# Kernel optimization log

Hardware: AMD Instinct MI355X
Metric: run time of the kernel (lower is better)

## Reference

```python
import jax, jax.numpy as jnp
import numpy as np

DIM = 128; D_STATE = 16; D_CONV = 4; EXPAND = 2
D_INNER = DIM * EXPAND            # 256
DT_RANK = (DIM + 15) // 16        # 8
B, H, W = 2, 56, 56


def _ln(x, w, b):
    m = jnp.mean(x, -1, keepdims=True)
    v = jnp.var(x, -1, keepdims=True)
    return (x - m) * jax.lax.rsqrt(v + 1e-5) * w + b


def _mamba(x, in_w, conv_w, conv_b, xproj_w, dt_w, dt_b, A_log, Dp, out_w):
    # x: (B, L, DIM)
    Bb, L, _ = x.shape
    xz = x @ in_w.T                                   # (B,L,2*D_INNER)
    xi, z = jnp.split(xz, 2, axis=-1)
    # causal depthwise conv1d (pad left d_conv-1, truncate to L)
    xc = jnp.transpose(xi, (0, 2, 1))                 # (B,D_INNER,L)
    xc = jax.lax.conv_general_dilated(
        xc, conv_w, (1,), [(D_CONV - 1, 0)],
        dimension_numbers=('NCH', 'OIH', 'NCH'),
        feature_group_count=D_INNER) + conv_b[None, :, None]
    xs = jax.nn.silu(jnp.transpose(xc, (0, 2, 1)))    # (B,L,D_INNER)
    dbl = xs @ xproj_w.T                              # (B,L,DT_RANK+2*D_STATE)
    dt = jax.nn.softplus(dbl[..., :DT_RANK] @ dt_w.T + dt_b)   # (B,L,D_INNER)
    Bc = dbl[..., DT_RANK:DT_RANK + D_STATE]          # (B,L,D_STATE)
    Cc = dbl[..., DT_RANK + D_STATE:]                 # (B,L,D_STATE)
    A = -jnp.exp(A_log)                               # (D_INNER,D_STATE)
    dA = jnp.exp(dt[..., None] * A)                   # (B,L,D_INNER,D_STATE)
    dBu = (dt * xs)[..., None] * Bc[:, :, None, :]    # (B,L,D_INNER,D_STATE)

    def step(h, inp):
        a, bu, c = inp
        h = a * h + bu                                # (B,D_INNER,D_STATE)
        return h, jnp.einsum('bdn,bn->bd', h, c)

    h0 = jnp.zeros((Bb, D_INNER, D_STATE), x.dtype)
    _, ys = jax.lax.scan(step, h0, (jnp.moveaxis(dA, 1, 0),
                                    jnp.moveaxis(dBu, 1, 0),
                                    jnp.moveaxis(Cc, 1, 0)))
    y = jnp.moveaxis(ys, 0, 1) + xs * Dp              # (B,L,D_INNER)
    y = y * jax.nn.silu(z)
    return y @ out_w.T                                # (B,L,DIM)


def _forward(x, norm_h_w, norm_h_b, norm_v_w, norm_v_b,
             dw_w, dw_b, pw_w, pw_b,
             h_in_w, h_conv_w, h_conv_b, h_xproj_w, h_dt_w, h_dt_b, h_A_log, h_D, h_out_w,
             v_in_w, v_conv_w, v_conv_b, v_xproj_w, v_dt_w, v_dt_b, v_A_log, v_D, v_out_w,
             ca_fc1_w, ca_fc2_w):
    Bb, C, Hh, Ww = x.shape
    # local branch: depthwise 3x3 + GELU + 1x1
    lf = jax.lax.conv_general_dilated(
        x, dw_w, (1, 1), [(1, 1), (1, 1)],
        dimension_numbers=('NCHW', 'OIHW', 'NCHW'),
        feature_group_count=C) + dw_b[None, :, None, None]
    lf = jax.nn.gelu(lf, approximate=False)
    lf = jnp.einsum('bchw,oc->bohw', lf, pw_w[:, :, 0, 0]) + pw_b[None, :, None, None]
    # horizontal scan: row-major tokens
    xh = _ln(x.reshape(Bb, C, Hh * Ww).transpose(0, 2, 1), norm_h_w, norm_h_b)
    oh = _mamba(xh, h_in_w, h_conv_w, h_conv_b, h_xproj_w, h_dt_w, h_dt_b,
                h_A_log, h_D, h_out_w)
    oh = oh.transpose(0, 2, 1).reshape(Bb, C, Hh, Ww)
    # vertical scan: column-major tokens
    xv = _ln(jnp.transpose(x, (0, 1, 3, 2)).reshape(Bb, C, Ww * Hh).transpose(0, 2, 1),
             norm_v_w, norm_v_b)
    ov = _mamba(xv, v_in_w, v_conv_w, v_conv_b, v_xproj_w, v_dt_w, v_dt_b,
                v_A_log, v_D, v_out_w)
    ov = jnp.transpose(ov.transpose(0, 2, 1).reshape(Bb, C, Ww, Hh), (0, 1, 3, 2))
    fused = oh + ov + lf
    # channel attention
    y = jnp.mean(fused, axis=(2, 3))                  # (B,C)
    y = jax.nn.sigmoid(jax.nn.relu(y @ ca_fc1_w.T) @ ca_fc2_w.T)
    return fused * y[:, :, None, None] + x


def setup_inputs() -> dict:
    key = jax.random.key(0)
    ks = iter(jax.random.split(key, 64))
    def nrm(shape, scale):
        return jax.random.normal(next(ks), shape, jnp.float32) * scale
    d = {}
    d['x'] = nrm((B, DIM, H, W), 1.0)
    d['norm_h_w'] = jnp.ones((DIM,), jnp.float32); d['norm_h_b'] = jnp.zeros((DIM,), jnp.float32)
    d['norm_v_w'] = jnp.ones((DIM,), jnp.float32); d['norm_v_b'] = jnp.zeros((DIM,), jnp.float32)
    d['dw_w'] = nrm((DIM, 1, 3, 3), 1.0 / 3.0)
    d['dw_b'] = jnp.zeros((DIM,), jnp.float32)
    d['pw_w'] = nrm((DIM, DIM, 1, 1), DIM ** -0.5)
    d['pw_b'] = jnp.zeros((DIM,), jnp.float32)
    for p in ('h', 'v'):
        d[p + '_in_w'] = nrm((2 * D_INNER, DIM), DIM ** -0.5)
        d[p + '_conv_w'] = nrm((D_INNER, 1, D_CONV), D_CONV ** -0.5)
        d[p + '_conv_b'] = jnp.zeros((D_INNER,), jnp.float32)
        d[p + '_xproj_w'] = nrm((DT_RANK + 2 * D_STATE, D_INNER), D_INNER ** -0.5)
        d[p + '_dt_w'] = nrm((D_INNER, DT_RANK), DT_RANK ** -0.5)
        d[p + '_dt_b'] = jnp.full((D_INNER,), -2.0, jnp.float32)  # small positive dt
        d[p + '_A_log'] = jnp.log(jnp.tile(jnp.arange(1, D_STATE + 1, dtype=jnp.float32), (D_INNER, 1)))
        d[p + '_D'] = jnp.ones((D_INNER,), jnp.float32)
        d[p + '_out_w'] = nrm((DIM, D_INNER), D_INNER ** -0.5)
    d['ca_fc1_w'] = nrm((DIM // 4, DIM), DIM ** -0.5)
    d['ca_fc2_w'] = nrm((DIM, DIM // 4), (DIM // 4) ** -0.5)
    return d


def reference(x, norm_h_w, norm_h_b, norm_v_w, norm_v_b,
              dw_w, dw_b, pw_w, pw_b,
              h_in_w, h_conv_w, h_conv_b, h_xproj_w, h_dt_w, h_dt_b, h_A_log, h_D, h_out_w,
              v_in_w, v_conv_w, v_conv_b, v_xproj_w, v_dt_w, v_dt_b, v_A_log, v_D, v_out_w,
              ca_fc1_w, ca_fc2_w):
    return _forward(x, norm_h_w, norm_h_b, norm_v_w, norm_v_b,
                    dw_w, dw_b, pw_w, pw_b,
                    h_in_w, h_conv_w, h_conv_b, h_xproj_w, h_dt_w, h_dt_b, h_A_log, h_D, h_out_w,
                    v_in_w, v_conv_w, v_conv_b, v_xproj_w, v_dt_w, v_dt_b, v_A_log, v_D, v_out_w,
                    ca_fc1_w, ca_fc2_w)
```

## Files before the change

kernel.cpp:

```cpp
#include <hip/hip_runtime.h>
#include <hip/hip_bf16.h>

typedef __hip_bfloat16 bf16;
__device__ __forceinline__ float b2f(bf16 v){ return __bfloat162float(v); }
__device__ __forceinline__ bf16 f2b(float v){ return __float2bfloat16(v); }

typedef __attribute__((ext_vector_type(8))) short frag_ab;
typedef __attribute__((ext_vector_type(4))) float frag_cd;
typedef __attribute__((ext_vector_type(4))) short short4v;

__device__ __forceinline__ frag_ab ld_frag_2xb64(const bf16* p){
  union { frag_ab f; short4v h[2]; } u;
  u.h[0] = *reinterpret_cast<const short4v*>(p);
  u.h[1] = *reinterpret_cast<const short4v*>(p+4);
  return u.f;
}

#define LLEN 3136
#define BATCH 2
#define NCHUNK 49
#define LC 64

__global__ void k_front(const float* __restrict__ x, const float* __restrict__ dww,
                        const float* __restrict__ dwb, bf16* __restrict__ tmp,
                        const float* nhw_, const float* nhb_, const float* nvw_,
                        const float* nvb_, bf16* __restrict__ xln,
                        float* __restrict__ YMEAN){
  int blk = blockIdx.x;
  int tid = threadIdx.x;
  if (blk < 1024){
    int bc = blk & 255;
    int seg = blk >> 8;
    int c = bc & 127;
    if (bc == 0 && seg == 0 && tid < 256) YMEAN[tid] = 0.f;
    const float* xp = x + (size_t)bc*LLEN;
    float w[9];
    #pragma unroll
    for (int i=0;i<9;i++) w[i] = dww[c*9+i];
    float bias = dwb[c];
    int pstart = seg * 784;
    for (int p = pstart + tid; p < pstart + 784; p += 256){
      int i = p/56, j = p%56;
      float acc = bias;
      #pragma unroll
      for (int a=0;a<3;a++){
        int ii = i + a - 1;
        if (ii < 0 || ii >= 56) continue;
        #pragma unroll
        for (int bb=0;bb<3;bb++){
          int jj = j + bb - 1;
          if (jj < 0 || jj >= 56) continue;
          acc += w[a*3+bb] * xp[ii*56+jj];
        }
      }
      float g = 0.5f*acc*(1.0f + erff(acc*0.70710678118654752f));
      tmp[(size_t)bc*LLEN + p] = f2b(g);
    }
  } else {
    int idx2 = blk - 1024;
    int h = idx2 % 56, b = idx2 / 56;
    __shared__ float sx[128][57];
    __shared__ float smean[56], srstd[56];
    __shared__ float wh[128], bh[128], wv_[128], bv_[128];
    if (tid < 128){ wh[tid]=nhw_[tid]; bh[tid]=nhb_[tid];
                    wv_[tid]=nvw_[tid]; bv_[tid]=nvb_[tid]; }
    for (int idx = tid; idx < 128*56; idx += 256){
      int c = idx / 56, w = idx % 56;
      sx[c][w] = x[((size_t)(b*128+c))*LLEN + h*56 + w];
    }
    __syncthreads();
    if (tid < 56){
      float s=0.f, s2=0.f;
      for (int c=0;c<128;c++){ float v = sx[c][tid]; s+=v; s2+=v*v; }
      float m = s*(1.f/128.f);
      float var = s2*(1.f/128.f) - m*m;
      smean[tid]=m; srstd[tid]=rsqrtf(var+1e-5f);
    }
    __syncthreads();
    bf16* outh = xln;
    bf16* outv = xln + (size_t)BATCH*LLEN*128;
    for (int idx = tid; idx < 56*128; idx += 256){
      int w = idx >> 7, c = idx & 127;
      float v = (sx[c][w]-smean[w])*srstd[w];
      outh[((size_t)b*LLEN + h*56 + w)*128 + c] = f2b(v*wh[c]+bh[c]);
      outv[((size_t)b*LLEN + w*56 + h)*128 + c] = f2b(v*wv_[c]+bv_[c]);
    }
  }
}

__global__ void k_inproj(const bf16* __restrict__ xln, const float* __restrict__ hw,
                         const float* __restrict__ vw, bf16* __restrict__ XI, bf16* __restrict__ Z){
  int dir = blockIdx.z;
  const bf16* A = xln + (size_t)dir*BATCH*LLEN*128;
  const float* W = dir ? vw : hw;
  int m0 = blockIdx.x*64;
  int npair = blockIdx.y*128;
  __shared__ __align__(16) bf16 sA[64][136];
  __shared__ __align__(16) bf16 sW[64][136];
  int tid = threadIdx.x;
  #pragma unroll
  for (int r=0;r<4;r++){
    int idx = tid + r*256;
    int row = idx >> 4, c8 = (idx & 15)*8;
    *reinterpret_cast<float4*>(&sA[row][c8]) =
        *reinterpret_cast<const float4*>(&A[(size_t)(m0+row)*128 + c8]);
  }
  int wv2 = tid >> 6, lane = tid & 63;
  int qd = lane >> 4, mr = lane & 15;
  bf16* dst = (npair < 256) ? XI : Z;
  int nbase0 = npair & 255;
  size_t dslab = (size_t)dir*BATCH*LLEN*256;
  #pragma unroll
  for (int nt=0; nt<2; nt++){
    int n0 = npair + nt*64;
    __syncthreads();
    #pragma unroll
    for (int r=0;r<8;r++){
      int idx = tid + r*256;
      int row = idx >> 5, c4 = (idx & 31)*4;
      float4 w4 = *reinterpret_cast<const float4*>(&W[(size_t)(n0+row)*128 + c4]);
      bf16 t4[4] = {f2b(w4.x), f2b(w4.y), f2b(w4.z), f2b(w4.w)};
      *reinterpret_cast<double*>(&sW[row][c4]) = *reinterpret_cast<double*>(t4);
    }
    __syncthreads();
    frag_cd acc[4] = {};
    #pragma unroll
    for (int k0=0;k0<128;k0+=32){
      frag_ab af = *reinterpret_cast<frag_ab*>(&sA[wv2*16+mr][k0+qd*8]);
      #pragma unroll
      for (int t=0;t<4;t++){
        frag_ab bfr = *reinterpret_cast<frag_ab*>(&sW[t*16+mr][k0+qd*8]);
        acc[t] = __builtin_amdgcn_mfma_f32_16x16x32_bf16(af, bfr, acc[t], 0, 0, 0);
      }
    }
    int nb = nbase0 + nt*64;
    #pragma unroll
    for (int t=0;t<4;t++)
      #pragma unroll
      for (int r=0;r<4;r++){
        int row = m0 + wv2*16 + qd*4 + r;
        int col = nb + t*16 + mr;
        dst[dslab + (size_t)row*256 + col] = f2b(acc[t][r]);
      }
  }
}

__global__ void k_conv(const bf16* __restrict__ XI, const float* hw, const float* hb,
                       const float* vw, const float* vb, bf16* __restrict__ XS2){
  int dir = blockIdx.z;
  int b = blockIdx.y;
  int bd = dir*BATCH + b;
  int l0 = blockIdx.x * 32;
  const bf16* XId = XI + (size_t)bd*LLEN*256;
  const float* cw = dir ? vw : hw;
  const float* cb = dir ? vb : hb;
  __shared__ float sxi[35][256];
  int tid = threadIdx.x;
  for (int r = 0; r < 35; r++){
    int l = l0 - 3 + r;
    sxi[r][tid] = (l >= 0) ? b2f(XId[(size_t)l*256 + tid]) : 0.f;
  }
  __syncthreads();
  float w0=cw[tid*4], w1=cw[tid*4+1], w2=cw[tid*4+2], w3=cw[tid*4+3];
  float bias = cb[tid];
  size_t x2base = ((size_t)bd*16 + (tid>>4))*LLEN;
  int c16 = tid & 15;
  for (int ll=0; ll<32; ll++){
    float acc = bias + w0*sxi[ll][tid] + w1*sxi[ll+1][tid] + w2*sxi[ll+2][tid] + w3*sxi[ll+3][tid];
    float s = acc / (1.f + __expf(-acc));
    XS2[(x2base + l0 + ll)*16 + c16] = f2b(s);
  }
}

__global__ void k_dbl(const bf16* __restrict__ XS2, const float* __restrict__ hx,
                      const float* __restrict__ vx,
                      const float* hdw, const float* vdw, const float* hdb, const float* vdb,
                      bf16* __restrict__ DT2, float* __restrict__ Bf, float* __restrict__ Cf){
  int m0 = blockIdx.x*64;
  int bd = m0 / LLEN;
  int l0m = m0 % LLEN;
  int dirq = bd >> 1;
  const float* W = dirq ? vx : hx;
  __shared__ __align__(16) bf16 sA[64][264];
  __shared__ __align__(16) bf16 sW[48][264];
  __shared__ float sdbl[64][49];
  int tid = threadIdx.x;
  #pragma unroll
  for (int r=0;r<8;r++){
    int idx = tid + r*256;
    int row = idx >> 5, c8 = (idx & 31)*8;
    size_t src = (((size_t)bd*16 + (c8>>4))*LLEN + l0m + row)*16 + (c8&15);
    *reinterpret_cast<float4*>(&sA[row][c8]) =
        *reinterpret_cast<const float4*>(&XS2[src]);
  }
  #pragma unroll
  for (int r=0;r<12;r++){
    int idx = tid + r*256;
    int row = idx >> 6, c4 = (idx & 63)*4;
    bf16 t4[4] = {f2b(0.f), f2b(0.f), f2b(0.f), f2b(0.f)};
    if (row < 40){
      float4 w4 = *reinterpret_cast<const float4*>(&W[(size_t)row*256 + c4]);
      t4[0]=f2b(w4.x); t4[1]=f2b(w4.y); t4[2]=f2b(w4.z); t4[3]=f2b(w4.w);
    }
    *reinterpret_cast<double*>(&sW[row][c4]) = *reinterpret_cast<double*>(t4);
  }
  __syncthreads();
  int wv2 = tid >> 6, lane = tid & 63;
  int qd = lane >> 4, mr = lane & 15;
  frag_cd acc[3] = {};
  #pragma unroll
  for (int k0=0;k0<256;k0+=32){
    frag_ab af = *reinterpret_cast<frag_ab*>(&sA[wv2*16+mr][k0+qd*8]);
    #pragma unroll
    for (int t=0;t<3;t++){
      frag_ab bfr = *reinterpret_cast<frag_ab*>(&sW[t*16+mr][k0+qd*8]);
      acc[t] = __builtin_amdgcn_mfma_f32_16x16x32_bf16(af, bfr, acc[t], 0, 0, 0);
    }
  }
  #pragma unroll
  for (int t=0;t<3;t++)
    #pragma unroll
    for (int r=0;r<4;r++){
      int col = t*16 + mr;
      if (col < 40) sdbl[wv2*16 + qd*4 + r][col] = acc[t][r];
    }
  __syncthreads();
  const float* dtw = dirq ? vdw : hdw;
  const float* dtb = dirq ? vdb : hdb;
  float w8[8];
  #pragma unroll
  for (int r=0;r<8;r++) w8[r] = dtw[tid*8+r];
  float biasv = dtb[tid];
  size_t d2base = ((size_t)bd*16 + (tid>>4))*LLEN + l0m;
  int c16 = tid & 15;
  for (int row=0; row<64; row++){
    float a = biasv;
    #pragma unroll
    for (int r=0;r<8;r++) a += sdbl[row][r]*w8[r];
    float sv = (a > 20.f) ? a : __logf(1.f + __expf(a));
    DT2[(d2base + row)*16 + c16] = f2b(sv);
  }
  #pragma unroll
  for (int r=0;r<8;r++){
    int idx = tid + r*256;
    int row = idx >> 5, o = idx & 31;
    float v = sdbl[row][8+o];
    size_t rr = (size_t)(m0+row)*16;
    if (o < 16) Bf[rr + o] = v;
    else        Cf[rr + (o-16)] = v;
  }
}

__global__ void k_scan1(const bf16* __restrict__ DT2, const bf16* __restrict__ XS2,
                        const float* __restrict__ Bc, const float* hA, const float* vA,
                        float* __restrict__ Pbuf, float* __restrict__ Hbuf){
  int bd = blockIdx.z;
  int g  = blockIdx.y;
  int ck = blockIdx.x;
  int l0 = ck*LC;
  const float* Bd = Bc + (size_t)bd*LLEN*16;
  const float* Alog = (bd >> 1) ? vA : hA;
  int tid = threadIdx.x;
  int dl = tid >> 4, n = tid & 15;
  float A = -__expf(Alog[(g*16+dl)*16+n]);
  __shared__ float sdt[LC][16], sxs[LC][16], sB[LC][16];
  size_t base2 = (((size_t)bd*16 + g)*LLEN + l0)*16;
  #pragma unroll
  for (int r=0;r<4;r++){
    int idx = tid + r*256;
    sdt[idx>>4][idx&15] = b2f(DT2[base2 + idx]);
    sxs[idx>>4][idx&15] = b2f(XS2[base2 + idx]);
    (&sB[0][0])[idx] = Bd[(size_t)l0*16 + idx];
  }
  __syncthreads();
  float h = 0.f, P = 1.f;
  #pragma unroll 8
  for (int i=0;i<LC;i++){
    float a = sdt[i][dl];
    float u = sxs[i][dl];
    float dA = __expf(a * A);
    h = dA*h + (a*u)*sB[i][n];
    P *= dA;
  }
  size_t sidx = (((size_t)bd*16 + g)*NCHUNK + ck)*256 + tid;
  Pbuf[sidx] = P;
  Hbuf[sidx] = h;
}

__global__ void k_scan2(const float* __restrict__ Pbuf, float* __restrict__ Hbuf){
  int q = blockIdx.x;
  int tid = threadIdx.x;
  float carry = 0.f;
  for (int k=0;k<NCHUNK;k++){
    size_t idx = ((size_t)q*NCHUNK + k)*256 + tid;
    float Pv = Pbuf[idx];
    float He = Hbuf[idx];
    Hbuf[idx] = carry;
    carry = Pv*carry + He;
  }
}

__global__ void k_scan3(const bf16* __restrict__ DT2, const bf16* __restrict__ XS2,
                        const float* __restrict__ Bc, const float* __restrict__ Cc,
                        const float* hA, const float* vA,
                        const float* __restrict__ Hbuf, bf16* __restrict__ ys){
  int bd = blockIdx.z;
  int g  = blockIdx.y;
  int ck = blockIdx.x;
  int l0 = ck*LC;
  const float* Bd = Bc + (size_t)bd*LLEN*16;
  const float* Cd = Cc + (size_t)bd*LLEN*16;
  bf16* yd = ys + (size_t)bd*LLEN*256;
  const float* Alog = (bd >> 1) ? vA : hA;
  int tid = threadIdx.x;
  int dl = tid >> 4, n = tid & 15;
  float A = -__expf(Alog[(g*16+dl)*16+n]);
  __shared__ float sdt[LC][16], sxs[LC][16], sB[LC][16], sC[LC][16];
  __shared__ float sp2[16][272];
  size_t base2 = (((size_t)bd*16 + g)*LLEN + l0)*16;
  #pragma unroll
  for (int r=0;r<4;r++){
    int idx = tid + r*256;
    sdt[idx>>4][idx&15] = b2f(DT2[base2 + idx]);
    sxs[idx>>4][idx&15] = b2f(XS2[base2 + idx]);
    (&sB[0][0])[idx] = Bd[(size_t)l0*16 + idx];
    (&sC[0][0])[idx] = Cd[(size_t)l0*16 + idx];
  }
  size_t sidx = (((size_t)bd*16 + g)*NCHUNK + ck)*256 + tid;
  float h = Hbuf[sidx];
  __syncthreads();
  int swz = dl*17 + n;
  int i_local = tid >> 4;
  int c16 = tid & 15;
  int rbase = c16*17;
  for (int i0=0; i0<LC; i0+=16){
    #pragma unroll
    for (int ii=0;ii<16;ii++){
      int i = i0 + ii;
      float a = sdt[i][dl];
      float u = sxs[i][dl];
      float dA = __expf(a * A);
      h = dA*h + (a*u)*sB[i][n];
      sp2[ii][swz] = h * sC[i][n];
    }
    __syncthreads();
    const float* row = &sp2[i_local][rbase];
    float s = 0.f;
    #pragma unroll
    for (int k=0;k<16;k++) s += row[k];
    yd[(size_t)(l0+i0+i_local)*256 + g*16 + c16] = f2b(s);
    __syncthreads();
  }
}

__global__ void k_outgemm(const bf16* __restrict__ ys, const bf16* __restrict__ XS2,
                          const bf16* __restrict__ Z, const float* __restrict__ hD,
                          const float* __restrict__ vD, const float* __restrict__ how,
                          const float* __restrict__ vow, bf16* __restrict__ OD){
  int dir = blockIdx.y;
  size_t slab = (size_t)dir*BATCH*LLEN*256;
  const float* W = dir ? vow : how;
  const float* Dw = dir ? vD : hD;
  bf16* od = OD + (size_t)dir*BATCH*LLEN*128;
  int m0 = blockIdx.x*32;
  int bd = dir*2 + m0/LLEN;
  int lbase = m0 % LLEN;
  __shared__ __align__(16) bf16 sA[32][264];
  __shared__ __align__(16) bf16 sW[64][264];
  int tid = threadIdx.x;
  #pragma unroll
  for (int r=0;r<4;r++){
    int idx = tid + r*256;
    int row = idx >> 5, c8 = (idx & 31)*8;
    size_t e = slab + (size_t)(m0+row)*256 + c8;
    size_t e2 = (((size_t)bd*16 + (c8>>4))*LLEN + lbase + row)*16 + (c8&15);
    bf16 yb[8], xb[8], zb[8], ob[8];
    *reinterpret_cast<float4*>(yb) = *reinterpret_cast<const float4*>(&ys[e]);
    *reinterpret_cast<float4*>(xb) = *reinterpret_cast<const float4*>(&XS2[e2]);
    *reinterpret_cast<float4*>(zb) = *reinterpret_cast<const float4*>(&Z[e]);
    #pragma unroll
    for (int j=0;j<8;j++){
      float Dv = Dw[c8 + j];
      float yv = b2f(yb[j]) + b2f(xb[j])*Dv;
      float zv = b2f(zb[j]);
      ob[j] = f2b(yv * (zv/(1.f+__expf(-zv))));
    }
    *reinterpret_cast<float4*>(&sA[row][c8]) = *reinterpret_cast<float4*>(ob);
  }
  int wv2 = tid >> 6, lane = tid & 63;
  int qd = lane >> 4, mr = lane & 15;
  int msub = wv2 & 1, tpair = (wv2 >> 1)*2;
  #pragma unroll
  for (int nh=0; nh<2; nh++){
    int n0 = nh*64;
    __syncthreads();
    #pragma unroll
    for (int r=0;r<16;r++){
      int idx = tid + r*256;
      int row = idx >> 6, c4 = (idx & 63)*4;
      float4 w4 = *reinterpret_cast<const float4*>(&W[(size_t)(n0+row)*256 + c4]);
      bf16 t4[4] = {f2b(w4.x), f2b(w4.y), f2b(w4.z), f2b(w4.w)};
      *reinterpret_cast<double*>(&sW[row][c4]) = *reinterpret_cast<double*>(t4);
    }
    __syncthreads();
    frag_cd acc[2] = {};
    #pragma unroll
    for (int k0=0;k0<256;k0+=32){
      frag_ab af = *reinterpret_cast<frag_ab*>(&sA[msub*16+mr][k0+qd*8]);
      #pragma unroll
      for (int i=0;i<2;i++){
        frag_ab bfr = *reinterpret_cast<frag_ab*>(&sW[(tpair+i)*16+mr][k0+qd*8]);
        acc[i] = __builtin_amdgcn_mfma_f32_16x16x32_bf16(af, bfr, acc[i], 0, 0, 0);
      }
    }
    #pragma unroll
    for (int i=0;i<2;i++)
      #pragma unroll
      for (int r=0;r<4;r++){
        int row = m0 + msub*16 + qd*4 + r;
        int col = n0 + (tpair+i)*16 + mr;
        od[(size_t)row*128 + col] = f2b(acc[i][r]);
      }
  }
}

__global__ void k_pwcomb(const bf16* __restrict__ tmp, const float* __restrict__ pww,
                         const float* __restrict__ pwb, const bf16* __restrict__ OD,
                         float* __restrict__ fused, float* __restrict__ YMEAN){
  int p0 = blockIdx.x * 64;
  int m0 = blockIdx.y * 64;
  int b  = blockIdx.z;
  const bf16* T = tmp + (size_t)b*128*LLEN;
  const bf16* od0 = OD + (size_t)b*LLEN*128;
  const bf16* od1 = OD + (size_t)(BATCH + b)*LLEN*128;
  __shared__ __align__(16) bf16 sA[64][136];
  __shared__ __align__(16) bf16 sBt[64][132];
  __shared__ float sOD[64][65];
  int tid = threadIdx.x;
  #pragma unroll
  for (int r=0;r<8;r++){
    int idx = tid + r*256;
    int row = idx >> 5, c4 = (idx & 31)*4;
    float4 w4 = *reinterpret_cast<const float4*>(&pww[(size_t)(m0+row)*128 + c4]);
    bf16 t4[4] = {f2b(w4.x), f2b(w4.y), f2b(w4.z), f2b(w4.w)};
    *reinterpret_cast<double*>(&sA[row][c4]) = *reinterpret_cast<double*>(t4);
  }
  #pragma unroll
  for (int r=0;r<8;r++){
    int idx = tid + r*256;
    int c = idx >> 4, p4 = (idx & 15)*4;
    union { double d; bf16 v[4]; } u;
    u.d = *reinterpret_cast<const double*>(&T[(size_t)c*LLEN + p0 + p4]);
    #pragma unroll
    for (int j=0;j<4;j++) sBt[p4+j][c] = u.v[j];
  }
  #pragma unroll
  for (int r=0;r<8;r++){
    int idx = tid + r*256;
    int prow = idx >> 5, mp = (idx & 31)*2;
    int p = p0 + prow;
    int pi = p/56, pj = p%56;
    int pt = pj*56 + pi;
    bf16 a0[2], a1[2];
    *reinterpret_cast<float*>(a0) = *reinterpret_cast<const float*>(&od0[(size_t)p*128 + m0 + mp]);
    *reinterpret_cast<float*>(a1) = *reinterpret_cast<const float*>(&od1[(size_t)pt*128 + m0 + mp]);
    sOD[prow][mp]   = b2f(a0[0]) + b2f(a1[0]);
    sOD[prow][mp+1] = b2f(a0[1]) + b2f(a1[1]);
  }
  __syncthreads();
  int wv2 = tid >> 6, lane = tid & 63;
  int qd = lane >> 4, mr = lane & 15;
  frag_cd acc[4] = {};
  #pragma unroll
  for (int k0=0;k0<128;k0+=32){
    frag_ab af = *reinterpret_cast<frag_ab*>(&sA[wv2*16+mr][k0+qd*8]);
    #pragma unroll
    for (int t=0;t<4;t++){
      frag_ab bfr = ld_frag_2xb64(&sBt[t*16+mr][k0+qd*8]);
      acc[t] = __builtin_amdgcn_mfma_f32_16x16x32_bf16(af, bfr, acc[t], 0, 0, 0);
    }
  }
  #pragma unroll
  for (int r=0;r<4;r++){
    int m = m0 + wv2*16 + qd*4 + r;
    float bias = pwb[m];
    float s = 0.f;
    #pragma unroll
    for (int t=0;t<4;t++){
      int p = p0 + t*16 + mr;
      float val = acc[t][r] + bias + sOD[t*16+mr][m - m0];
      fused[((size_t)b*128 + m)*LLEN + p] = val;
      s += val;
    }
    s += __shfl_xor(s, 1, 16);
    s += __shfl_xor(s, 2, 16);
    s += __shfl_xor(s, 4, 16);
    s += __shfl_xor(s, 8, 16);
    if (mr == 0) atomicAdd(&YMEAN[b*128 + m], s);
  }
}

__global__ void k_final_gate(const float* __restrict__ fused, const float* __restrict__ YMEAN,
                             const float* __restrict__ fc1, const float* __restrict__ fc2,
                             const float* __restrict__ x, float* __restrict__ out){
  int bc = blockIdx.y;
  int b = bc >> 7, c = bc & 127;
  __shared__ float ym[128], s1[32];
  __shared__ float gsh;
  int tid = threadIdx.x;
  if (tid < 128) ym[tid] = YMEAN[b*128 + tid] * (1.f/(float)LLEN);
  __syncthreads();
  if (tid < 32){
    float a = 0.f;
    for (int cc=0;cc<128;cc++) a += ym[cc]*fc1[tid*128+cc];
    s1[tid] = fmaxf(a, 0.f);
  }
  __syncthreads();
  if (tid == 0){
    float a = 0.f;
    #pragma unroll
    for (int j=0;j<32;j++) a += s1[j]*fc2[c*32+j];
    gsh = 1.f/(1.f+__expf(-a));
  }
  __syncthreads();
  float g = gsh;
  int p = blockIdx.x*256 + tid;
  if (p < LLEN){
    size_t i = (size_t)bc*LLEN + p;
    out[i] = fused[i]*g + x[i];
  }
}

extern "C" void kernel_launch(void* const* d_in, const int* in_sizes, int n_in,
                              void* d_out, int out_size, void* d_ws, size_t ws_size,
                              hipStream_t stream) {
  const float* x      = (const float*)d_in[0];
  const float* nhw    = (const float*)d_in[1];
  const float* nhb    = (const float*)d_in[2];
  const float* nvw    = (const float*)d_in[3];
  const float* nvb    = (const float*)d_in[4];
  const float* dww    = (const float*)d_in[5];
  const float* dwb    = (const float*)d_in[6];
  const float* pww    = (const float*)d_in[7];
  const float* pwb    = (const float*)d_in[8];
  const float* h_inw  = (const float*)d_in[9];
  const float* h_cw   = (const float*)d_in[10];
  const float* h_cb   = (const float*)d_in[11];
  const float* h_xw   = (const float*)d_in[12];
  const float* h_dtw  = (const float*)d_in[13];
  const float* h_dtb  = (const float*)d_in[14];
  const float* h_Al   = (const float*)d_in[15];
  const float* h_D    = (const float*)d_in[16];
  const float* h_ow   = (const float*)d_in[17];
  const float* v_inw  = (const float*)d_in[18];
  const float* v_cw   = (const float*)d_in[19];
  const float* v_cb   = (const float*)d_in[20];
  const float* v_xw   = (const float*)d_in[21];
  const float* v_dtw  = (const float*)d_in[22];
  const float* v_dtb  = (const float*)d_in[23];
  const float* v_Al   = (const float*)d_in[24];
  const float* v_D    = (const float*)d_in[25];
  const float* v_ow   = (const float*)d_in[26];
  const float* fc1    = (const float*)d_in[27];
  const float* fc2    = (const float*)d_in[28];

  float* FUSED = (float*)d_out;
  float* out   = (float*)d_out;

  char* base = (char*)d_ws;
  bf16*  XLN   = (bf16*)(base + 1605632);
  bf16*  DT2   = (bf16*)(base + 0);
  bf16*  OD    = (bf16*)(base + 0);
  bf16*  XI    = (bf16*)(base + 6422528);
  bf16*  YS    = (bf16*)(base + 6422528);
  bf16*  Z     = (bf16*)(base + 12845056);
  bf16*  XS2   = (bf16*)(base + 19267584);
  float* Bf    = (float*)(base + 25690112);
  float* Cf    = (float*)(base + 26492928);
  float* Hbuf  = (float*)(base + 27295744);
  float* YMEAN = (float*)(base + 30507008);
  bf16*  TMP   = (bf16*)(base + 30508032);
  float* Pbuf  = (float*)(base + 32113664);

  k_front<<<dim3(1024 + 56*BATCH), dim3(256), 0, stream>>>(x, dww, dwb, TMP,
                                                           nhw, nhb, nvw, nvb, XLN, YMEAN);
  k_inproj<<<dim3(98,4,2), dim3(256), 0, stream>>>(XLN, h_inw, v_inw, XI, Z);
  k_conv<<<dim3(98,BATCH,2), dim3(256), 0, stream>>>(XI, h_cw, h_cb, v_cw, v_cb, XS2);
  k_dbl<<<dim3(196), dim3(256), 0, stream>>>(XS2, h_xw, v_xw, h_dtw, v_dtw, h_dtb, v_dtb,
                                             DT2, Bf, Cf);
  k_scan1<<<dim3(NCHUNK,16,4), dim3(256), 0, stream>>>(DT2, XS2, Bf, h_Al, v_Al, Pbuf, Hbuf);
  k_scan2<<<dim3(64), dim3(256), 0, stream>>>(Pbuf, Hbuf);
  k_scan3<<<dim3(NCHUNK,16,4), dim3(256), 0, stream>>>(DT2, XS2, Bf, Cf, h_Al, v_Al, Hbuf, YS);
  k_outgemm<<<dim3(196,2), dim3(256), 0, stream>>>(YS, XS2, Z, h_D, v_D, h_ow, v_ow, OD);
  k_pwcomb<<<dim3(49,2,BATCH), dim3(256), 0, stream>>>(TMP, pww, pwb, OD, FUSED, YMEAN);
  k_final_gate<<<dim3(13,256), dim3(256), 0, stream>>>(FUSED, YMEAN, fc1, fc2, x, out);
}
```

Baseline: 237.5 us.

## Fuse causal conv+SiLU into x-projection GEMM and restructure final gate kernel

```diff
diff --git a/kernel.cpp b/kernel.cpp
--- a/kernel.cpp
+++ b/kernel.cpp
@@ -145,53 +145,30 @@
   }
 }
 
-__global__ void k_conv(const bf16* __restrict__ XI, const float* hw, const float* hb,
-                       const float* vw, const float* vb, bf16* __restrict__ XS2){
-  int dir = blockIdx.z;
-  int b = blockIdx.y;
-  int bd = dir*BATCH + b;
-  int l0 = blockIdx.x * 32;
-  const bf16* XId = XI + (size_t)bd*LLEN*256;
-  const float* cw = dir ? vw : hw;
-  const float* cb = dir ? vb : hb;
-  __shared__ float sxi[35][256];
-  int tid = threadIdx.x;
-  for (int r = 0; r < 35; r++){
-    int l = l0 - 3 + r;
-    sxi[r][tid] = (l >= 0) ? b2f(XId[(size_t)l*256 + tid]) : 0.f;
-  }
-  __syncthreads();
-  float w0=cw[tid*4], w1=cw[tid*4+1], w2=cw[tid*4+2], w3=cw[tid*4+3];
-  float bias = cb[tid];
-  size_t x2base = ((size_t)bd*16 + (tid>>4))*LLEN;
-  int c16 = tid & 15;
-  for (int ll=0; ll<32; ll++){
-    float acc = bias + w0*sxi[ll][tid] + w1*sxi[ll+1][tid] + w2*sxi[ll+2][tid] + w3*sxi[ll+3][tid];
-    float s = acc / (1.f + __expf(-acc));
-    XS2[(x2base + l0 + ll)*16 + c16] = f2b(s);
-  }
-}
-
-__global__ void k_dbl(const bf16* __restrict__ XS2, const float* __restrict__ hx,
-                      const float* __restrict__ vx,
+__global__ void k_dbl(const bf16* __restrict__ XI,
+                      const float* hcw, const float* hcb, const float* vcw, const float* vcb,
+                      const float* __restrict__ hx, const float* __restrict__ vx,
                       const float* hdw, const float* vdw, const float* hdb, const float* vdb,
-                      bf16* __restrict__ DT2, float* __restrict__ Bf, float* __restrict__ Cf){
+                      bf16* __restrict__ XS2, bf16* __restrict__ DT2,
+                      float* __restrict__ Bf, float* __restrict__ Cf){
   int m0 = blockIdx.x*64;
   int bd = m0 / LLEN;
   int l0m = m0 % LLEN;
   int dirq = bd >> 1;
+  const bf16* XId = XI + (size_t)bd*LLEN*256;
   const float* W = dirq ? vx : hx;
-  __shared__ __align__(16) bf16 sA[64][264];
+  const float* cw = dirq ? vcw : hcw;
+  const float* cb = dirq ? vcb : hcb;
+  __shared__ __align__(16) bf16 sA[67][264];
   __shared__ __align__(16) bf16 sW[48][264];
   __shared__ float sdbl[64][49];
   int tid = threadIdx.x;
-  #pragma unroll
-  for (int r=0;r<8;r++){
-    int idx = tid + r*256;
+  for (int idx = tid; idx < 67*32; idx += 256){
     int row = idx >> 5, c8 = (idx & 31)*8;
-    size_t src = (((size_t)bd*16 + (c8>>4))*LLEN + l0m + row)*16 + (c8&15);
-    *reinterpret_cast<float4*>(&sA[row][c8]) =
-        *reinterpret_cast<const float4*>(&XS2[src]);
+    int l = l0m - 3 + row;
+    float4 v = make_float4(0.f,0.f,0.f,0.f);
+    if (l >= 0) v = *reinterpret_cast<const float4*>(&XId[(size_t)l*256 + c8]);
+    *reinterpret_cast<float4*>(&sA[row][c8]) = v;
   }
   #pragma unroll
   for (int r=0;r<12;r++){
@@ -203,6 +180,24 @@
       t4[0]=f2b(w4.x); t4[1]=f2b(w4.y); t4[2]=f2b(w4.z); t4[3]=f2b(w4.w);
     }
     *reinterpret_cast<double*>(&sW[row][c4]) = *reinterpret_cast<double*>(t4);
+  }
+  __syncthreads();
+  {
+    float w0=cw[tid*4], w1=cw[tid*4+1], w2=cw[tid*4+2], w3=cw[tid*4+3];
+    float cbias = cb[tid];
+    size_t x2base = ((size_t)bd*16 + (tid>>4))*LLEN + l0m;
+    int c16 = tid & 15;
+    float xm3 = b2f(sA[0][tid]), xm2 = b2f(sA[1][tid]), xm1 = b2f(sA[2][tid]);
+    #pragma unroll 4
+    for (int j=0;j<64;j++){
+      float x0 = b2f(sA[j+3][tid]);
+      float acc = cbias + w0*xm3 + w1*xm2 + w2*xm1 + w3*x0;
+      float s = acc / (1.f + __expf(-acc));
+      bf16 sv = f2b(s);
+      sA[j][tid] = sv;
+      XS2[(x2base + j)*16 + c16] = sv;
+      xm3=xm2; xm2=xm1; xm1=x0;
+    }
   }
   __syncthreads();
   int wv2 = tid >> 6, lane = tid & 63;
@@ -291,6 +286,7 @@
   int q = blockIdx.x;
   int tid = threadIdx.x;
   float carry = 0.f;
+  #pragma unroll 7
   for (int k=0;k<NCHUNK;k++){
     size_t idx = ((size_t)q*NCHUNK + k)*256 + tid;
     float Pv = Pbuf[idx];
@@ -503,31 +499,45 @@
 __global__ void k_final_gate(const float* __restrict__ fused, const float* __restrict__ YMEAN,
                              const float* __restrict__ fc1, const float* __restrict__ fc2,
                              const float* __restrict__ x, float* __restrict__ out){
-  int bc = blockIdx.y;
+  int bc = blockIdx.x;
   int b = bc >> 7, c = bc & 127;
   __shared__ float ym[128], s1[32];
   __shared__ float gsh;
   int tid = threadIdx.x;
   if (tid < 128) ym[tid] = YMEAN[b*128 + tid] * (1.f/(float)LLEN);
   __syncthreads();
+  {
+    int o = tid >> 3, part = tid & 7;
+    float a = 0.f;
+    #pragma unroll
+    for (int k=0;k<16;k++) a += ym[part*16 + k] * fc1[o*128 + part*16 + k];
+    a += __shfl_xor(a, 1, 8);
+    a += __shfl_xor(a, 2, 8);
+    a += __shfl_xor(a, 4, 8);
+    if (part == 0) s1[o] = fmaxf(a, 0.f);
+  }
+  __syncthreads();
   if (tid < 32){
-    float a = 0.f;
-    for (int cc=0;cc<128;cc++) a += ym[cc]*fc1[tid*128+cc];
-    s1[tid] = fmaxf(a, 0.f);
-  }
-  __syncthreads();
-  if (tid == 0){
-    float a = 0.f;
-    #pragma unroll
-    for (int j=0;j<32;j++) a += s1[j]*fc2[c*32+j];
-    gsh = 1.f/(1.f+__expf(-a));
+    float a = s1[tid] * fc2[c*32 + tid];
+    a += __shfl_xor(a, 1, 32);
+    a += __shfl_xor(a, 2, 32);
+    a += __shfl_xor(a, 4, 32);
+    a += __shfl_xor(a, 8, 32);
+    a += __shfl_xor(a, 16, 32);
+    if (tid == 0) gsh = 1.f/(1.f+__expf(-a));
   }
   __syncthreads();
   float g = gsh;
-  int p = blockIdx.x*256 + tid;
-  if (p < LLEN){
-    size_t i = (size_t)bc*LLEN + p;
-    out[i] = fused[i]*g + x[i];
+  const float4* f4 = reinterpret_cast<const float4*>(fused) + (size_t)bc*784;
+  const float4* x4 = reinterpret_cast<const float4*>(x) + (size_t)bc*784;
+  float4* o4 = reinterpret_cast<float4*>(out) + (size_t)bc*784;
+  #pragma unroll
+  for (int it=0; it<4; it++){
+    int p = it*256 + tid;
+    if (p < 784){
+      float4 fv = f4[p], xv = x4[p];
+      o4[p] = make_float4(fv.x*g+xv.x, fv.y*g+xv.y, fv.z*g+xv.z, fv.w*g+xv.w);
+    }
   }
 }
 
@@ -585,13 +595,13 @@
   k_front<<<dim3(1024 + 56*BATCH), dim3(256), 0, stream>>>(x, dww, dwb, TMP,
                                                            nhw, nhb, nvw, nvb, XLN, YMEAN);
   k_inproj<<<dim3(98,4,2), dim3(256), 0, stream>>>(XLN, h_inw, v_inw, XI, Z);
-  k_conv<<<dim3(98,BATCH,2), dim3(256), 0, stream>>>(XI, h_cw, h_cb, v_cw, v_cb, XS2);
-  k_dbl<<<dim3(196), dim3(256), 0, stream>>>(XS2, h_xw, v_xw, h_dtw, v_dtw, h_dtb, v_dtb,
-                                             DT2, Bf, Cf);
+  k_dbl<<<dim3(196), dim3(256), 0, stream>>>(XI, h_cw, h_cb, v_cw, v_cb,
+                                             h_xw, v_xw, h_dtw, v_dtw, h_dtb, v_dtb,
+                                             XS2, DT2, Bf, Cf);
   k_scan1<<<dim3(NCHUNK,16,4), dim3(256), 0, stream>>>(DT2, XS2, Bf, h_Al, v_Al, Pbuf, Hbuf);
   k_scan2<<<dim3(64), dim3(256), 0, stream>>>(Pbuf, Hbuf);
   k_scan3<<<dim3(NCHUNK,16,4), dim3(256), 0, stream>>>(DT2, XS2, Bf, Cf, h_Al, v_Al, Hbuf, YS);
   k_outgemm<<<dim3(196,2), dim3(256), 0, stream>>>(YS, XS2, Z, h_D, v_D, h_ow, v_ow, OD);
   k_pwcomb<<<dim3(49,2,BATCH), dim3(256), 0, stream>>>(TMP, pww, pwb, OD, FUSED, YMEAN);
-  k_final_gate<<<dim3(13,256), dim3(256), 0, stream>>>(FUSED, YMEAN, fc1, fc2, x, out);
-}
+  k_final_gate<<<dim3(256), dim3(256), 0, stream>>>(FUSED, YMEAN, fc1, fc2, x, out);
+}
```

Measured after the change: 221.9 us. -6.6%, faster.
